# Performance work log

Hardware: AMD Instinct MI355X
Metric: run time of the kernel (lower is better)

## Reference

```python
import jax, jax.numpy as jnp
import numpy as np

BATCH = 4096
IN = 1024
HID = 1024
EPS = 1e-5


def _batch_norm(x, gamma, beta):
    # training-mode batch norm over the batch dim (biased variance, like
    # torch.nn.functional.batch_norm with training=True)
    mean = jnp.mean(x, axis=0)
    var = jnp.var(x, axis=0)
    return gamma * (x - mean) * jax.lax.rsqrt(var + EPS) + beta


def setup_inputs() -> dict:
    key = jax.random.key(0)
    ks = jax.random.split(key, 6)
    input_ = jax.random.normal(ks[0], (BATCH, IN), dtype=jnp.float32)
    h_0 = jax.random.normal(ks[1], (BATCH, HID), dtype=jnp.float32)
    c_0 = jax.random.normal(ks[2], (BATCH, HID), dtype=jnp.float32)
    weight_ih = jax.random.normal(ks[3], (IN, 4 * HID), dtype=jnp.float32) / np.sqrt(IN)
    weight_hh = jnp.tile(jnp.eye(HID, dtype=jnp.float32), (1, 4))
    bias = jnp.zeros((4 * HID,), dtype=jnp.float32)
    gamma_ih = jnp.full((4 * HID,), 0.1, dtype=jnp.float32)
    beta_ih = jnp.zeros((4 * HID,), dtype=jnp.float32)
    gamma_hh = jnp.full((4 * HID,), 0.1, dtype=jnp.float32)
    beta_hh = jnp.zeros((4 * HID,), dtype=jnp.float32)
    gamma_c = jnp.full((HID,), 0.1, dtype=jnp.float32)
    beta_c = jnp.zeros((HID,), dtype=jnp.float32)
    return {
        "input_": input_, "h_0": h_0, "c_0": c_0,
        "weight_ih": weight_ih, "weight_hh": weight_hh, "bias": bias,
        "gamma_ih": gamma_ih, "beta_ih": beta_ih,
        "gamma_hh": gamma_hh, "beta_hh": beta_hh,
        "gamma_c": gamma_c, "beta_c": beta_c,
        "time": 5,
    }


def reference(input_, h_0, c_0, weight_ih, weight_hh, bias,
              gamma_ih, beta_ih, gamma_hh, beta_hh, gamma_c, beta_c, time):
    # time selects per-timestep running stats; in training mode batch stats
    # are used so it does not affect the math.
    wh = h_0 @ weight_hh                     # [B, 4H]
    wi = input_ @ weight_ih                  # [B, 4H]
    bn_wh = _batch_norm(wh, gamma_hh, beta_hh)
    bn_wi = _batch_norm(wi, gamma_ih, beta_ih)
    pre = bn_wh + bn_wi + bias               # [B, 4H]
    f, i, o, g = jnp.split(pre, 4, axis=1)   # gate order f,i,o,g
    c_1 = jax.nn.sigmoid(f) * c_0 + jax.nn.sigmoid(i) * jnp.tanh(g)
    h_1 = jax.nn.sigmoid(o) * jnp.tanh(_batch_norm(c_1, gamma_c, beta_c))
    return h_1, c_1
```

## Files before the change

kernel.cpp:

```cpp
#include <hip/hip_runtime.h>
#include <math.h>

typedef __bf16 bf16;
typedef __bf16 bf16x8 __attribute__((ext_vector_type(8)));
typedef float  f32x4  __attribute__((ext_vector_type(4)));

#define BATCH 4096
#define HID   1024
#define FH    4096
#define KDIM  1024
#define EPS   1e-5f
#define NSTAT (4 * FH + 2 * HID)

__global__ __launch_bounds__(256) void prep_k(const float* __restrict__ w0,
                                              bf16* __restrict__ bt0,
                                              const float* __restrict__ w1,
                                              bf16* __restrict__ bt1,
                                              const float* __restrict__ x0,
                                              bf16* __restrict__ a0,
                                              const float* __restrict__ x1,
                                              bf16* __restrict__ a1,
                                              float* __restrict__ stats) {
  const int t = threadIdx.x;
  const int z = blockIdx.z;
  if (z < 2) {
    const float* src = z ? w1 : w0;
    bf16*        dst = z ? bt1 : bt0;
    __shared__ float tile[64][65];
    const int c0 = blockIdx.x * 64;
    const int r0 = blockIdx.y * 64;
#pragma unroll
    for (int i = 0; i < 4; ++i) {
      int r = (t >> 4) + i * 16;
      int c = (t & 15) * 4;
      float4 v = *(const float4*)(src + (size_t)(r0 + r) * FH + c0 + c);
      tile[r][c] = v.x; tile[r][c + 1] = v.y;
      tile[r][c + 2] = v.z; tile[r][c + 3] = v.w;
    }
    __syncthreads();
#pragma unroll
    for (int j = 0; j < 2; ++j) {
      int n = (t >> 3) + j * 32;
      int k = (t & 7) * 8;
      bf16x8 o;
#pragma unroll
      for (int e = 0; e < 8; ++e) o[e] = (bf16)tile[k + e][n];
      *(bf16x8*)(dst + (size_t)(c0 + n) * KDIM + r0 + k) = o;
    }
  } else {
    const float* src = (z == 2) ? x0 : x1;
    bf16*        dst = (z == 2) ? a0 : a1;
    size_t base = ((size_t)(blockIdx.y * 64 + blockIdx.x) * 256 + t) * 16;
#pragma unroll
    for (int h = 0; h < 2; ++h) {
      float4 v0 = *(const float4*)(src + base + h * 8);
      float4 v1 = *(const float4*)(src + base + h * 8 + 4);
      bf16x8 o;
      o[0] = (bf16)v0.x; o[1] = (bf16)v0.y; o[2] = (bf16)v0.z; o[3] = (bf16)v0.w;
      o[4] = (bf16)v1.x; o[5] = (bf16)v1.y; o[6] = (bf16)v1.z; o[7] = (bf16)v1.w;
      *(bf16x8*)(dst + base + h * 8) = o;
    }
    if (z == 2 && blockIdx.x == 0 && blockIdx.y == 0) {
      for (int i = t; i < NSTAT; i += 256) stats[i] = 0.f;
    }
  }
}

#define BM 128
#define BN 128
#define BKK 64

__device__ __forceinline__ void gload_lds16(const bf16* g, bf16* l) {
  __builtin_amdgcn_global_load_lds(
      (const __attribute__((address_space(1))) void*)g,
      (__attribute__((address_space(3))) void*)l, 16, 0, 0);
}

__global__ __launch_bounds__(256) void gemm_k(const bf16* __restrict__ A0,
                                              const bf16* __restrict__ Bt0,
                                              bf16* __restrict__ C0,
                                              const bf16* __restrict__ A1,
                                              const bf16* __restrict__ Bt1,
                                              bf16* __restrict__ C1,
                                              float* __restrict__ stats) {
  const bf16* A  = blockIdx.z ? A1 : A0;
  const bf16* Bt = blockIdx.z ? Bt1 : Bt0;
  bf16*       C  = blockIdx.z ? C1 : C0;
  float* sum = stats + (blockIdx.z ? 2 * FH : 0);
  float* ssq = sum + FH;

  __shared__ bf16 lA[BM * BKK];
  __shared__ bf16 lB[BN * BKK];

  const int t     = threadIdx.x;
  const int lane  = t & 63;
  const int w     = t >> 6;
  const int wm    = w >> 1, wn = w & 1;
  const int m0    = blockIdx.y * BM;
  const int n0    = blockIdx.x * BN;
  const int cidx  = lane & 15;
  const int quad  = lane >> 4;
  const int wbase = t & ~63;

  f32x4 acc[4][4] = {};

  for (int kc = 0; kc < KDIM; kc += BKK) {
#pragma unroll
    for (int q = 0; q < 4; ++q) {
      int idx = q * 256 + t;
      int r   = idx >> 3;
      int pc  = idx & 7;
      int lc  = pc ^ (r & 7);
      const bf16* ga = A  + (size_t)(m0 + r) * KDIM + kc + lc * 8;
      const bf16* gb = Bt + (size_t)(n0 + r) * KDIM + kc + lc * 8;
      bf16* ldst = lA + (size_t)(q * 256 + wbase) * 8;
      gload_lds16(ga, ldst);
      gload_lds16(gb, lB + (size_t)(q * 256 + wbase) * 8);
    }
    __syncthreads();
#pragma unroll
    for (int ks = 0; ks < 2; ++ks) {
      bf16x8 af[4], bfr[4];
#pragma unroll
      for (int mt = 0; mt < 4; ++mt) {
        int row = wm * 64 + mt * 16 + cidx;
        int ch  = (ks * 4 + quad) ^ (row & 7);
        af[mt] = *(const bf16x8*)(lA + row * BKK + ch * 8);
      }
#pragma unroll
      for (int nt = 0; nt < 4; ++nt) {
        int row = wn * 64 + nt * 16 + cidx;
        int ch  = (ks * 4 + quad) ^ (row & 7);
        bfr[nt] = *(const bf16x8*)(lB + row * BKK + ch * 8);
      }
#pragma unroll
      for (int mt = 0; mt < 4; ++mt)
#pragma unroll
        for (int nt = 0; nt < 4; ++nt)
          acc[mt][nt] = __builtin_amdgcn_mfma_f32_16x16x32_bf16(
              af[mt], bfr[nt], acc[mt][nt], 0, 0, 0);
    }
    __syncthreads();
  }

#pragma unroll
  for (int mt = 0; mt < 4; ++mt) {
#pragma unroll
    for (int r = 0; r < 4; ++r) {
      int row = m0 + wm * 64 + mt * 16 + quad * 4 + r;
      bf16* crow = C + (size_t)row * FH + n0 + wn * 64 + cidx;
#pragma unroll
      for (int nt = 0; nt < 4; ++nt)
        crow[nt * 16] = (bf16)acc[mt][nt][r];
    }
  }

#pragma unroll
  for (int nt = 0; nt < 4; ++nt) {
    float s = 0.f, q = 0.f;
#pragma unroll
    for (int mt = 0; mt < 4; ++mt)
#pragma unroll
      for (int r = 0; r < 4; ++r) {
        float v = acc[mt][nt][r];
        s += v;
        q += v * v;
      }
    s += __shfl_xor(s, 16, 64);
    s += __shfl_xor(s, 32, 64);
    q += __shfl_xor(q, 16, 64);
    q += __shfl_xor(q, 32, 64);
    if (quad == 0) {
      int col = n0 + wn * 64 + nt * 16 + cidx;
      atomicAdd(&sum[col], s);
      atomicAdd(&ssq[col], q);
    }
  }
}

__device__ __forceinline__ float rcpf(float x) { return __builtin_amdgcn_rcpf(x); }
__device__ __forceinline__ float sigf(float x) { return rcpf(1.f + __expf(-x)); }
__device__ __forceinline__ float tanh_f(float x) {
  return 1.f - 2.f * rcpf(__expf(2.f * x) + 1.f);
}
__device__ __forceinline__ float bflo(unsigned u) {
  union { unsigned x; float f; } v; v.x = u << 16; return v.f;
}
__device__ __forceinline__ float bfhi(unsigned u) {
  union { unsigned x; float f; } v; v.x = u & 0xffff0000u; return v.f;
}

__global__ __launch_bounds__(256) void gates_k(const bf16* __restrict__ wi,
                                               const bf16* __restrict__ wh,
                                               const float* __restrict__ c0p,
                                               const float* __restrict__ bias,
                                               const float* __restrict__ g_ih,
                                               const float* __restrict__ b_ih,
                                               const float* __restrict__ g_hh,
                                               const float* __restrict__ b_hh,
                                               const float* __restrict__ stats,
                                               float* __restrict__ statsc,
                                               float* __restrict__ c1_out,
                                               float* __restrict__ sig_o) {
  const int jp = blockIdx.x * 256 + threadIdx.x;
  const int j  = jp * 2;
  const int r0 = blockIdx.y * 16;
  const float inv = 1.f / (float)BATCH;
  float sI[4][2], sH[4][2], cc[4][2];
#pragma unroll
  for (int g = 0; g < 4; ++g)
#pragma unroll
    for (int e = 0; e < 2; ++e) {
      int col  = j + e + g * HID;
      float mi = stats[col] * inv;
      float vi = stats[FH + col] * inv - mi * mi;
      float ri = rsqrtf(vi + EPS);
      float mh = stats[2 * FH + col] * inv;
      float vh = stats[3 * FH + col] * inv - mh * mh;
      float rh = rsqrtf(vh + EPS);
      sI[g][e] = g_ih[col] * ri;
      sH[g][e] = g_hh[col] * rh;
      cc[g][e] = b_ih[col] - mi * sI[g][e] + b_hh[col] - mh * sH[g][e] + bias[col];
    }
  const unsigned* wiu = (const unsigned*)wi;
  const unsigned* whu = (const unsigned*)wh;
  const float2*   c02 = (const float2*)c0p;
  float2* c12 = (float2*)c1_out;
  float2* so2 = (float2*)sig_o;
  float sc[2] = {0.f, 0.f}, qc[2] = {0.f, 0.f};
#pragma unroll 4
  for (int r = 0; r < 16; ++r) {
    size_t row = (size_t)(r0 + r);
    size_t b2  = row * (FH / 2) + jp;
    unsigned ui[4], uh[4];
#pragma unroll
    for (int g = 0; g < 4; ++g) {
      ui[g] = wiu[b2 + g * (HID / 2)];
      uh[g] = whu[b2 + g * (HID / 2)];
    }
    float2 c0v = c02[row * (HID / 2) + jp];
    float2 c1v, sov;
    {
      float pf = sI[0][0] * bflo(ui[0]) + sH[0][0] * bflo(uh[0]) + cc[0][0];
      float pi = sI[1][0] * bflo(ui[1]) + sH[1][0] * bflo(uh[1]) + cc[1][0];
      float po = sI[2][0] * bflo(ui[2]) + sH[2][0] * bflo(uh[2]) + cc[2][0];
      float pg = sI[3][0] * bflo(ui[3]) + sH[3][0] * bflo(uh[3]) + cc[3][0];
      c1v.x = sigf(pf) * c0v.x + sigf(pi) * tanh_f(pg);
      sov.x = sigf(po);
    }
    {
      float pf = sI[0][1] * bfhi(ui[0]) + sH[0][1] * bfhi(uh[0]) + cc[0][1];
      float pi = sI[1][1] * bfhi(ui[1]) + sH[1][1] * bfhi(uh[1]) + cc[1][1];
      float po = sI[2][1] * bfhi(ui[2]) + sH[2][1] * bfhi(uh[2]) + cc[2][1];
      float pg = sI[3][1] * bfhi(ui[3]) + sH[3][1] * bfhi(uh[3]) + cc[3][1];
      c1v.y = sigf(pf) * c0v.y + sigf(pi) * tanh_f(pg);
      sov.y = sigf(po);
    }
    c12[row * (HID / 2) + jp] = c1v;
    so2[row * (HID / 2) + jp] = sov;
    sc[0] += c1v.x; qc[0] += c1v.x * c1v.x;
    sc[1] += c1v.y; qc[1] += c1v.y * c1v.y;
  }
  atomicAdd(&statsc[j], sc[0]);
  atomicAdd(&statsc[j + 1], sc[1]);
  atomicAdd(&statsc[HID + j], qc[0]);
  atomicAdd(&statsc[HID + j + 1], qc[1]);
}

__global__ __launch_bounds__(256) void hout_k(const float* __restrict__ c1_in,
                                              const float* __restrict__ sig_o,
                                              const float* __restrict__ g_c,
                                              const float* __restrict__ b_c,
                                              const float* __restrict__ statsc,
                                              float* __restrict__ h_out) {
  const int t  = threadIdx.x;
  const int r0 = blockIdx.y * 16;
  const float inv = 1.f / (float)BATCH;
  float sc[4], sh[4];
#pragma unroll
  for (int e = 0; e < 4; ++e) {
    int j   = t * 4 + e;
    float m = statsc[j] * inv;
    float v = statsc[HID + j] * inv - m * m;
    float rs = rsqrtf(v + EPS);
    sc[e] = g_c[j] * rs;
    sh[e] = b_c[j] - m * sc[e];
  }
  const float4* c14 = (const float4*)c1_in;
  const float4* so4 = (const float4*)sig_o;
  float4* h4 = (float4*)h_out;
#pragma unroll 4
  for (int r = 0; r < 16; ++r) {
    size_t idx = (size_t)(r0 + r) * (HID / 4) + t;
    float4 c1 = c14[idx];
    float4 so = so4[idx];
    float4 hv;
    hv.x = so.x * tanh_f(sc[0] * c1.x + sh[0]);
    hv.y = so.y * tanh_f(sc[1] * c1.y + sh[1]);
    hv.z = so.z * tanh_f(sc[2] * c1.z + sh[2]);
    hv.w = so.w * tanh_f(sc[3] * c1.w + sh[3]);
    h4[idx] = hv;
  }
}

extern "C" void kernel_launch(void* const* d_in, const int* in_sizes, int n_in,
                              void* d_out, int out_size, void* d_ws,
                              size_t ws_size, hipStream_t stream) {
  const float* input_ = (const float*)d_in[0];
  const float* h0     = (const float*)d_in[1];
  const float* c0     = (const float*)d_in[2];
  const float* w_ih   = (const float*)d_in[3];
  const float* w_hh   = (const float*)d_in[4];
  const float* bias   = (const float*)d_in[5];
  const float* g_ih   = (const float*)d_in[6];
  const float* b_ih   = (const float*)d_in[7];
  const float* g_hh   = (const float*)d_in[8];
  const float* b_hh   = (const float*)d_in[9];
  const float* g_c    = (const float*)d_in[10];
  const float* b_c    = (const float*)d_in[11];

  char* ws = (char*)d_ws;
  bf16* bt_ih = (bf16*)(ws);
  bf16* bt_hh = (bf16*)(ws + (size_t)( 8u << 20));
  bf16* a_i   = (bf16*)(ws + (size_t)(16u << 20));
  bf16* a_h   = (bf16*)(ws + (size_t)(24u << 20));
  bf16* wi    = (bf16*)(ws + (size_t)(32u << 20));
  bf16* wh    = (bf16*)(ws + (size_t)(64u << 20));
  float* stats  = (float*)(ws + (size_t)(96u << 20));
  float* statsc = stats + 4 * FH;

  float* h_out  = (float*)d_out;
  float* c1_out = (float*)d_out + (size_t)BATCH * HID;
  float* sigo   = h_out;

  prep_k<<<dim3(64, 16, 4), 256, 0, stream>>>(
      w_ih, bt_ih, w_hh, bt_hh, input_, a_i, h0, a_h, stats);

  gemm_k<<<dim3(FH / BN, BATCH / BM, 2), 256, 0, stream>>>(
      a_i, bt_ih, wi, a_h, bt_hh, wh, stats);

  gates_k<<<dim3(2, BATCH / 16), 256, 0, stream>>>(
      wi, wh, c0, bias, g_ih, b_ih, g_hh, b_hh, stats, statsc, c1_out, sigo);

  hout_k<<<dim3(1, BATCH / 16), 256, 0, stream>>>(
      c1_out, sigo, g_c, b_c, statsc, h_out);
}
```

Baseline: 265.7 us.

## Fuse gates and output kernels using a grid-wide atomic barrier

```diff
diff --git a/kernel.cpp b/kernel.cpp
--- a/kernel.cpp
+++ b/kernel.cpp
@@ -11,6 +11,7 @@
 #define KDIM  1024
 #define EPS   1e-5f
 #define NSTAT (4 * FH + 2 * HID)
+#define GH_BLOCKS 512
 
 __global__ __launch_bounds__(256) void prep_k(const float* __restrict__ w0,
                                               bf16* __restrict__ bt0,
@@ -61,7 +62,7 @@
       *(bf16x8*)(dst + base + h * 8) = o;
     }
     if (z == 2 && blockIdx.x == 0 && blockIdx.y == 0) {
-      for (int i = t; i < NSTAT; i += 256) stats[i] = 0.f;
+      for (int i = t; i < NSTAT + 1; i += 256) stats[i] = 0.f;
     }
   }
 }
@@ -113,8 +114,7 @@
       int lc  = pc ^ (r & 7);
       const bf16* ga = A  + (size_t)(m0 + r) * KDIM + kc + lc * 8;
       const bf16* gb = Bt + (size_t)(n0 + r) * KDIM + kc + lc * 8;
-      bf16* ldst = lA + (size_t)(q * 256 + wbase) * 8;
-      gload_lds16(ga, ldst);
+      gload_lds16(ga, lA + (size_t)(q * 256 + wbase) * 8);
       gload_lds16(gb, lB + (size_t)(q * 256 + wbase) * 8);
     }
     __syncthreads();
@@ -190,7 +190,7 @@
   union { unsigned x; float f; } v; v.x = u & 0xffff0000u; return v.f;
 }
 
-__global__ __launch_bounds__(256) void gates_k(const bf16* __restrict__ wi,
+__global__ __launch_bounds__(256, 2) void gh_k(const bf16* __restrict__ wi,
                                                const bf16* __restrict__ wh,
                                                const float* __restrict__ c0p,
                                                const float* __restrict__ bias,
@@ -198,14 +198,19 @@
                                                const float* __restrict__ b_ih,
                                                const float* __restrict__ g_hh,
                                                const float* __restrict__ b_hh,
+                                               const float* __restrict__ g_c,
+                                               const float* __restrict__ b_c,
                                                const float* __restrict__ stats,
                                                float* __restrict__ statsc,
+                                               unsigned* __restrict__ bar,
                                                float* __restrict__ c1_out,
-                                               float* __restrict__ sig_o) {
-  const int jp = blockIdx.x * 256 + threadIdx.x;
-  const int j  = jp * 2;
-  const int r0 = blockIdx.y * 16;
+                                               float* __restrict__ h_out) {
+  const int bid = blockIdx.x;
+  const int jp  = (bid & 1) * 256 + threadIdx.x;
+  const int j   = jp * 2;
+  const int r0  = (bid >> 1) * 16;
   const float inv = 1.f / (float)BATCH;
+
   float sI[4][2], sH[4][2], cc[4][2];
 #pragma unroll
   for (int g = 0; g < 4; ++g)
@@ -222,13 +227,16 @@
       sH[g][e] = g_hh[col] * rh;
       cc[g][e] = b_ih[col] - mi * sI[g][e] + b_hh[col] - mh * sH[g][e] + bias[col];
     }
+
   const unsigned* wiu = (const unsigned*)wi;
   const unsigned* whu = (const unsigned*)wh;
   const float2*   c02 = (const float2*)c0p;
   float2* c12 = (float2*)c1_out;
-  float2* so2 = (float2*)sig_o;
+  float2* h2  = (float2*)h_out;
+
+  float2 c1r[16], sor[16];
   float sc[2] = {0.f, 0.f}, qc[2] = {0.f, 0.f};
-#pragma unroll 4
+#pragma unroll
   for (int r = 0; r < 16; ++r) {
     size_t row = (size_t)(r0 + r);
     size_t b2  = row * (FH / 2) + jp;
@@ -257,7 +265,8 @@
       sov.y = sigf(po);
     }
     c12[row * (HID / 2) + jp] = c1v;
-    so2[row * (HID / 2) + jp] = sov;
+    c1r[r] = c1v;
+    sor[r] = sov;
     sc[0] += c1v.x; qc[0] += c1v.x * c1v.x;
     sc[1] += c1v.y; qc[1] += c1v.y * c1v.y;
   }
@@ -265,41 +274,34 @@
   atomicAdd(&statsc[j + 1], sc[1]);
   atomicAdd(&statsc[HID + j], qc[0]);
   atomicAdd(&statsc[HID + j + 1], qc[1]);
-}
-
-__global__ __launch_bounds__(256) void hout_k(const float* __restrict__ c1_in,
-                                              const float* __restrict__ sig_o,
-                                              const float* __restrict__ g_c,
-                                              const float* __restrict__ b_c,
-                                              const float* __restrict__ statsc,
-                                              float* __restrict__ h_out) {
-  const int t  = threadIdx.x;
-  const int r0 = blockIdx.y * 16;
-  const float inv = 1.f / (float)BATCH;
-  float sc[4], sh[4];
-#pragma unroll
-  for (int e = 0; e < 4; ++e) {
-    int j   = t * 4 + e;
-    float m = statsc[j] * inv;
-    float v = statsc[HID + j] * inv - m * m;
-    float rs = rsqrtf(v + EPS);
-    sc[e] = g_c[j] * rs;
-    sh[e] = b_c[j] - m * sc[e];
-  }
-  const float4* c14 = (const float4*)c1_in;
-  const float4* so4 = (const float4*)sig_o;
-  float4* h4 = (float4*)h_out;
-#pragma unroll 4
+
+  __syncthreads();
+  if (threadIdx.x == 0) {
+    __hip_atomic_fetch_add(bar, 1u, __ATOMIC_ACQ_REL, __HIP_MEMORY_SCOPE_AGENT);
+    while (__hip_atomic_load(bar, __ATOMIC_ACQUIRE, __HIP_MEMORY_SCOPE_AGENT) <
+           (unsigned)GH_BLOCKS)
+      __builtin_amdgcn_s_sleep(8);
+  }
+  __syncthreads();
+
+  float scb[2], shb[2];
+#pragma unroll
+  for (int e = 0; e < 2; ++e) {
+    float m = __hip_atomic_load(&statsc[j + e], __ATOMIC_ACQUIRE,
+                                __HIP_MEMORY_SCOPE_AGENT) * inv;
+    float q = __hip_atomic_load(&statsc[HID + j + e], __ATOMIC_ACQUIRE,
+                                __HIP_MEMORY_SCOPE_AGENT) * inv;
+    float rs = rsqrtf(q - m * m + EPS);
+    scb[e] = g_c[j + e] * rs;
+    shb[e] = b_c[j + e] - m * scb[e];
+  }
+#pragma unroll
   for (int r = 0; r < 16; ++r) {
-    size_t idx = (size_t)(r0 + r) * (HID / 4) + t;
-    float4 c1 = c14[idx];
-    float4 so = so4[idx];
-    float4 hv;
-    hv.x = so.x * tanh_f(sc[0] * c1.x + sh[0]);
-    hv.y = so.y * tanh_f(sc[1] * c1.y + sh[1]);
-    hv.z = so.z * tanh_f(sc[2] * c1.z + sh[2]);
-    hv.w = so.w * tanh_f(sc[3] * c1.w + sh[3]);
-    h4[idx] = hv;
+    size_t row = (size_t)(r0 + r);
+    float2 hv;
+    hv.x = sor[r].x * tanh_f(scb[0] * c1r[r].x + shb[0]);
+    hv.y = sor[r].y * tanh_f(scb[1] * c1r[r].y + shb[1]);
+    h2[row * (HID / 2) + jp] = hv;
   }
 }
 
@@ -328,10 +330,10 @@
   bf16* wh    = (bf16*)(ws + (size_t)(64u << 20));
   float* stats  = (float*)(ws + (size_t)(96u << 20));
   float* statsc = stats + 4 * FH;
+  unsigned* bar = (unsigned*)(stats + NSTAT);
 
   float* h_out  = (float*)d_out;
   float* c1_out = (float*)d_out + (size_t)BATCH * HID;
-  float* sigo   = h_out;
 
   prep_k<<<dim3(64, 16, 4), 256, 0, stream>>>(
       w_ih, bt_ih, w_hh, bt_hh, input_, a_i, h0, a_h, stats);
@@ -339,9 +341,7 @@
   gemm_k<<<dim3(FH / BN, BATCH / BM, 2), 256, 0, stream>>>(
       a_i, bt_ih, wi, a_h, bt_hh, wh, stats);
 
-  gates_k<<<dim3(2, BATCH / 16), 256, 0, stream>>>(
-      wi, wh, c0, bias, g_ih, b_ih, g_hh, b_hh, stats, statsc, c1_out, sigo);
-
-  hout_k<<<dim3(1, BATCH / 16), 256, 0, stream>>>(
-      c1_out, sigo, g_c, b_c, statsc, h_out);
-}
+  gh_k<<<dim3(GH_BLOCKS), 256, 0, stream>>>(
+      wi, wh, c0, bias, g_ih, b_ih, g_hh, b_hh, g_c, b_c,
+      stats, statsc, bar, c1_out, h_out);
+}
```

After: 356.4 us. +34.1%, slower.
